# Kernel optimization log

Hardware: AMD Instinct MI355X
Metric: run time of the kernel (lower is better)

Reference implementation:

```python
import jax, jax.numpy as jnp
import numpy as np

N = 100000
E = 1600000
IN = 128
HID = 128
OUT = 40
EPS = 1e-5
NEG_SLOPE = 0.2


def _gat_layer(x, src, dst, W, a_src, a_dst, b, heads, out_dim):
    # x: [N, in]; W: [in, heads*out_dim]; a_src/a_dst: [heads, out_dim]; b: [heads*out_dim]
    n = x.shape[0]
    h = (x @ W).reshape(n, heads, out_dim)                      # [N, H, D]
    al_s = jnp.sum(h * a_src, axis=-1)                          # [N, H]
    al_d = jnp.sum(h * a_dst, axis=-1)                          # [N, H]
    e = jax.nn.leaky_relu(al_s[src] + al_d[dst], NEG_SLOPE)     # [E, H]
    m = jax.ops.segment_max(e, dst, num_segments=n)             # [N, H]
    m = jnp.where(jnp.isfinite(m), m, 0.0)
    ex = jnp.exp(e - m[dst])                                    # [E, H]
    denom = jax.ops.segment_sum(ex, dst, num_segments=n)        # [N, H]
    alpha = ex / (denom[dst] + 1e-16)                           # [E, H]
    out = jax.ops.segment_sum(alpha[:, :, None] * h[src], dst, num_segments=n)  # [N, H, D]
    return out.reshape(n, heads * out_dim) + b


def _bn(h, g, beta):
    mu = jnp.mean(h, axis=0)
    var = jnp.var(h, axis=0)
    return (h - mu) * jax.lax.rsqrt(var + EPS) * g + beta


def setup_inputs() -> dict:
    key = jax.random.key(0)
    ks = jax.random.split(key, 20)
    x = jax.random.normal(ks[0], (N, IN), dtype=jnp.float32)
    edge_index = jax.random.randint(ks[1], (2, E), 0, N, dtype=jnp.int64)
    s = 0.05
    d0 = HID // 2  # 64, heads=2
    return {
        "x": x,
        "edge_index": edge_index,
        "w0": jax.random.normal(ks[2], (IN, 2 * d0), jnp.float32) * s,
        "asrc0": jax.random.normal(ks[3], (2, d0), jnp.float32) * s,
        "adst0": jax.random.normal(ks[4], (2, d0), jnp.float32) * s,
        "b0": jnp.zeros((2 * d0,), jnp.float32),
        "g0": jnp.ones((2 * d0,), jnp.float32),
        "beta0": jnp.zeros((2 * d0,), jnp.float32),
        "w1": jax.random.normal(ks[5], (HID, 2 * d0), jnp.float32) * s,
        "asrc1": jax.random.normal(ks[6], (2, d0), jnp.float32) * s,
        "adst1": jax.random.normal(ks[7], (2, d0), jnp.float32) * s,
        "b1": jnp.zeros((2 * d0,), jnp.float32),
        "g1": jnp.ones((2 * d0,), jnp.float32),
        "beta1": jnp.zeros((2 * d0,), jnp.float32),
        "w2": jax.random.normal(ks[8], (HID, OUT), jnp.float32) * s,
        "asrc2": jax.random.normal(ks[9], (1, OUT), jnp.float32) * s,
        "adst2": jax.random.normal(ks[10], (1, OUT), jnp.float32) * s,
        "b2": jnp.zeros((OUT,), jnp.float32),
    }


def reference(x, edge_index, w0, asrc0, adst0, b0, g0, beta0,
              w1, asrc1, adst1, b1, g1, beta1,
              w2, asrc2, adst2, b2):
    src, dst = edge_index[0], edge_index[1]
    d0 = HID // 2
    # layer 0: GATConv(IN, 64, heads=2) -> BN -> ReLU (dropout off in eval)
    h = _gat_layer(x, src, dst, w0, asrc0, adst0, b0, 2, d0)
    h = jax.nn.relu(_bn(h, g0, beta0))
    # layer 1
    h = _gat_layer(h, src, dst, w1, asrc1, adst1, b1, 2, d0)
    h = jax.nn.relu(_bn(h, g1, beta1))
    # layer 2: GATConv(HID, OUT, heads=1), no bn/relu
    h = _gat_layer(h, src, dst, w2, asrc2, adst2, b2, 1, OUT)
    return h
```

## Files before the change

kernel.cpp:

```cpp
#include <hip/hip_runtime.h>
#include <cstdint>


#define TILE_A 8192
#define BCAP 10240
#define NSLICE 32

typedef __attribute__((ext_vector_type(8))) short bf16x8v;
typedef __attribute__((ext_vector_type(4))) float f32x4v;
typedef __attribute__((ext_vector_type(2))) float f32x2;
typedef __attribute__((ext_vector_type(2))) unsigned int u32x2;

__device__ __forceinline__ uint32_t bf16x2_pack(float a, float b) {
  uint32_t ua = __float_as_uint(a);
  ua = (ua + 0x7FFF + ((ua >> 16) & 1)) >> 16;
  uint32_t ub = __float_as_uint(b);
  ub = (ub + 0x7FFF + ((ub >> 16) & 1)) >> 16;
  return ua | (ub << 16);
}
__device__ __forceinline__ uint16_t bf16_1(float a) {
  uint32_t ua = __float_as_uint(a);
  return (uint16_t)((ua + 0x7FFF + ((ua >> 16) & 1)) >> 16);
}
__device__ __forceinline__ f32x2 up2(uint32_t u) {
  u32x2 t = {u << 16, u & 0xFFFF0000u};
  return __builtin_bit_cast(f32x2, t);
}


__global__ __launch_bounds__(256) void bucket_hist_k(const int* __restrict__ dst,
                                                     int* __restrict__ counts,
                                                     int E, int nbA, int nbuck) {
  __shared__ int hist[256];
  int t = threadIdx.x;
  hist[t] = 0;
  __syncthreads();
  int lo = blockIdx.x * TILE_A;
  int hi = min(lo + TILE_A, E);
  for (int i = lo + t; i < hi; i += 256) atomicAdd(&hist[dst[i] >> 9], 1);
  __syncthreads();
  if (t < nbuck) counts[t * nbA + blockIdx.x] = hist[t];
}

__global__ __launch_bounds__(1024) void scan_counts_k(int* __restrict__ counts, int M,
                                                      int* __restrict__ rowptr, int N, int E) {
  __shared__ int part[1024];
  int t = threadIdx.x;
  int chunk = (M + 1023) >> 10;
  int lo = t * chunk, hi = min(lo + chunk, M);
  int s = 0;
  for (int i = lo; i < hi; ++i) s += counts[i];
  part[t] = s;
  __syncthreads();
  for (int off = 1; off < 1024; off <<= 1) {
    int u = (t >= off) ? part[t - off] : 0;
    __syncthreads();
    part[t] += u;
    __syncthreads();
  }
  int run = (t == 0) ? 0 : part[t - 1];
  for (int i = lo; i < hi; ++i) {
    int v = counts[i];
    counts[i] = run;
    run += v;
  }
  if (t == 0) rowptr[N] = E;
}

__global__ __launch_bounds__(256) void bucket_scatter_k(const int* __restrict__ src,
                                                        const int* __restrict__ dst,
                                                        const int* __restrict__ counts,
                                                        uint32_t* __restrict__ barr,
                                                        int E, int nbA, int nbuck) {
  __shared__ int cur[256];
  int t = threadIdx.x;
  if (t < nbuck) cur[t] = counts[t * nbA + blockIdx.x];
  __syncthreads();
  int lo = blockIdx.x * TILE_A;
  int hi = min(lo + TILE_A, E);
  for (int i = lo + t; i < hi; i += 256) {
    int d = dst[i];
    int b = d >> 9;
    int pos = atomicAdd(&cur[b], 1);
    barr[pos] = ((uint32_t)(d & 511) << 17) | (uint32_t)src[i];
  }
}

__global__ __launch_bounds__(256) void bucket_sort_k(const uint32_t* __restrict__ barr,
                                                     const int* __restrict__ counts,
                                                     int* __restrict__ rowptr,
                                                     int* __restrict__ csr_src,
                                                     int nbA, int nbuck, int N, int E) {
  __shared__ uint32_t ebuf[BCAP];
  __shared__ int hist[512];
  __shared__ int cur[512];
  int b = blockIdx.x;
  int t = threadIdx.x;
  int start = counts[b * nbA];
  int end = (b == nbuck - 1) ? E : counts[(b + 1) * nbA];
  int cnt = end - start;
  if (cnt > BCAP) cnt = BCAP;
  for (int i = t; i < cnt; i += 256) ebuf[i] = barr[start + i];
  for (int i = t; i < 512; i += 256) hist[i] = 0;
  __syncthreads();
  for (int i = t; i < cnt; i += 256) atomicAdd(&hist[ebuf[i] >> 17], 1);
  __syncthreads();
  if (t < 64) {
    int v[8];
    int s = 0;
#pragma unroll
    for (int k = 0; k < 8; ++k) { v[k] = hist[t * 8 + k]; s += v[k]; }
    int inc = s;
#pragma unroll
    for (int off = 1; off < 64; off <<= 1) {
      int u = __shfl_up(inc, off, 64);
      if (t >= off) inc += u;
    }
    int run = inc - s;
#pragma unroll
    for (int k = 0; k < 8; ++k) { hist[t * 8 + k] = run; run += v[k]; }
  }
  __syncthreads();
  int node0 = b << 9;
  int lim = N - node0;
  if (lim > 512) lim = 512;
  for (int i = t; i < 512; i += 256) {
    cur[i] = hist[i];
    if (i < lim) rowptr[node0 + i] = start + hist[i];
  }
  __syncthreads();
  for (int i = t; i < cnt; i += 256) {
    uint32_t e = ebuf[i];
    int ld = e >> 17;
    int pos = atomicAdd(&cur[ld], 1);
    csr_src[start + pos] = (int)(e & 0x1FFFFu);
  }
}


__global__ void w_prep_all_k(const float* __restrict__ w0, const float* __restrict__ w1,
                             const float* __restrict__ w2, uint16_t* __restrict__ wt0,
                             uint16_t* __restrict__ wt1, uint16_t* __restrict__ wt2) {
  int idx = blockIdx.x * blockDim.x + threadIdx.x;
  if (idx < 16384) {
    int n = idx >> 7, k = idx & 127;
    wt0[idx] = bf16_1(w0[k * 128 + n]);
  } else if (idx < 32768) {
    int i = idx - 16384;
    int n = i >> 7, k = i & 127;
    wt1[i] = bf16_1(w1[k * 128 + n]);
  } else if (idx < 32768 + 48 * 128) {
    int i = idx - 32768;
    int n = i >> 7, k = i & 127;
    float v = (n < 40) ? w2[k * 40 + n] : 0.f;
    wt2[i] = bf16_1(v);
  }
}

template <bool NORM, int NT, int HEADS>
__global__ __launch_bounds__(256) void gemm_mfma_k(const float* __restrict__ X,
                                                   const uint16_t* __restrict__ WT,
                                                   uint16_t* __restrict__ Hout,
                                                   const float* __restrict__ stats,
                                                   const float* __restrict__ g,
                                                   const float* __restrict__ beta,
                                                   const float* __restrict__ asrc,
                                                   const float* __restrict__ adst,
                                                   float* __restrict__ als,
                                                   float* __restrict__ ald,
                                                   int nrows, int cols, int stride) {
  __shared__ short A_lds[64 * 136];
  __shared__ float sscale[128];
  __shared__ float sbias[128];
  int tid = threadIdx.x;
  if (NORM && tid < 128) {
    float s = 0.f, s2 = 0.f;
#pragma unroll 4
    for (int sl = 0; sl < NSLICE; ++sl) {
      s += stats[sl * 256 + tid];
      s2 += stats[sl * 256 + 128 + tid];
    }
    float invn = 1.0f / (float)nrows;
    float mean = s * invn;
    float var = s2 * invn - mean * mean;
    float sc = g[tid] * rsqrtf(var + 1e-5f);
    sscale[tid] = sc;
    sbias[tid] = beta[tid] - mean * sc;
  }
  if (NORM) __syncthreads();
  int row0 = blockIdx.x * 64;
#pragma unroll
  for (int it = 0; it < 8; ++it) {
    int e = (tid + it * 256) * 4;
    int row = e >> 7;
    int kh = e & 127;
    int gr = row0 + row;
    f32x4v xv = {0.f, 0.f, 0.f, 0.f};
    if (gr < nrows) xv = __builtin_nontemporal_load((const f32x4v*)(X + (size_t)gr * 128 + kh));
    if (NORM) {
      xv[0] = fmaxf(fmaf(xv[0], sscale[kh + 0], sbias[kh + 0]), 0.f);
      xv[1] = fmaxf(fmaf(xv[1], sscale[kh + 1], sbias[kh + 1]), 0.f);
      xv[2] = fmaxf(fmaf(xv[2], sscale[kh + 2], sbias[kh + 2]), 0.f);
      xv[3] = fmaxf(fmaf(xv[3], sscale[kh + 3], sbias[kh + 3]), 0.f);
    }
    uint2 pk;
    pk.x = bf16x2_pack(xv[0], xv[1]);
    pk.y = bf16x2_pack(xv[2], xv[3]);
    *(uint2*)(&A_lds[row * 136 + kh]) = pk;
  }
  __syncthreads();

  int wave = tid >> 6;
  int lane = tid & 63;
  int m = lane & 15;
  int quad = lane >> 4;

  bf16x8v afrag[4];
#pragma unroll
  for (int kc = 0; kc < 4; ++kc)
    afrag[kc] = *(const bf16x8v*)(&A_lds[(wave * 16 + m) * 136 + kc * 32 + quad * 8]);

  f32x4v acc[NT];
#pragma unroll
  for (int t = 0; t < NT; ++t) acc[t] = (f32x4v){0.f, 0.f, 0.f, 0.f};

#pragma unroll
  for (int t = 0; t < NT; ++t) {
#pragma unroll
    for (int kc = 0; kc < 4; ++kc) {
      bf16x8v bfrag = *(const bf16x8v*)(WT + ((t * 16 + m) * 128 + kc * 32 + quad * 8));
      acc[t] = __builtin_amdgcn_mfma_f32_16x16x32_bf16(afrag[kc], bfrag, acc[t], 0, 0, 0);
    }
  }

#pragma unroll
  for (int t = 0; t < NT; ++t) {
    int col = t * 16 + m;
    if (col >= cols) break;
#pragma unroll
    for (int r = 0; r < 4; ++r) {
      int row = row0 + wave * 16 + quad * 4 + r;
      if (row < nrows) Hout[(size_t)row * stride + col] = bf16_1(acc[t][r]);
    }
  }

  float as_v[NT], ad_v[NT];
#pragma unroll
  for (int t = 0; t < NT; ++t) {
    int col = t * 16 + m;
    as_v[t] = (col < cols) ? asrc[col] : 0.f;
    ad_v[t] = (col < cols) ? adst[col] : 0.f;
  }
#pragma unroll
  for (int r = 0; r < 4; ++r) {
    int row = row0 + wave * 16 + quad * 4 + r;
    if (HEADS == 2) {
      float s1h0 = 0.f, s2h0 = 0.f, s1h1 = 0.f, s2h1 = 0.f;
#pragma unroll
      for (int t = 0; t < NT / 2; ++t) {
        s1h0 += acc[t][r] * as_v[t];
        s2h0 += acc[t][r] * ad_v[t];
      }
#pragma unroll
      for (int t = NT / 2; t < NT; ++t) {
        s1h1 += acc[t][r] * as_v[t];
        s2h1 += acc[t][r] * ad_v[t];
      }
#pragma unroll
      for (int off = 1; off < 16; off <<= 1) {
        s1h0 += __shfl_xor(s1h0, off, 64);
        s2h0 += __shfl_xor(s2h0, off, 64);
        s1h1 += __shfl_xor(s1h1, off, 64);
        s2h1 += __shfl_xor(s2h1, off, 64);
      }
      if (m == 0 && row < nrows) {
        ((float2*)als)[row] = make_float2(s1h0, s1h1);
        ((float2*)ald)[row] = make_float2(s2h0, s2h1);
      }
    } else {
      float s1 = 0.f, s2 = 0.f;
#pragma unroll
      for (int t = 0; t < NT; ++t) {
        s1 += acc[t][r] * as_v[t];
        s2 += acc[t][r] * ad_v[t];
      }
#pragma unroll
      for (int off = 1; off < 16; off <<= 1) {
        s1 += __shfl_xor(s1, off, 64);
        s2 += __shfl_xor(s2, off, 64);
      }
      if (m == 0 && row < nrows) {
        als[row] = s1;
        ald[row] = s2;
      }
    }
  }
}

__global__ __launch_bounds__(256) void gat_gather2_k(const int* __restrict__ rowptr,
                                                     const int* __restrict__ csr_src,
                                                     const float* __restrict__ als,
                                                     const float* __restrict__ ald,
                                                     const uint16_t* __restrict__ H,
                                                     const float* __restrict__ bias,
                                                     float* __restrict__ out,
                                                     float* __restrict__ stats, int N) {
  __shared__ float red[4][256];
  int tid = threadIdx.x;
  int wv = tid >> 6;
  int n = blockIdx.x * 4 + wv;
  int lane = tid & 63;
  int slot = lane >> 4;
  int sub = lane & 15;
  int head = sub >> 3;
  bool alive = n < N;
  int start = 0, end = 0;
  float aldn = 0.f;
  if (alive) {
    start = rowptr[n];
    end = rowptr[n + 1];
    aldn = ald[2 * n + head];
  }
  const char* hbase = (const char*)H;
  uint32_t suboff = (uint32_t)sub << 4;
  bool dlane = (sub & 7) == 0;
  f32x2 acc0 = {0.f, 0.f}, acc1 = {0.f, 0.f}, acc2 = {0.f, 0.f}, acc3 = {0.f, 0.f};
  float dsum = 0.f;
  int j = start;
  for (; j + 16 <= end; j += 16) {
    int e0 = j + slot;
    int s0 = __builtin_nontemporal_load(csr_src + e0);
    int s1 = __builtin_nontemporal_load(csr_src + e0 + 4);
    int s2 = __builtin_nontemporal_load(csr_src + e0 + 8);
    int s3 = __builtin_nontemporal_load(csr_src + e0 + 12);
    uint4 u0 = *(const uint4*)(hbase + (((uint32_t)s0 << 8) + suboff));
    uint4 u1 = *(const uint4*)(hbase + (((uint32_t)s1 << 8) + suboff));
    uint4 u2 = *(const uint4*)(hbase + (((uint32_t)s2 << 8) + suboff));
    uint4 u3 = *(const uint4*)(hbase + (((uint32_t)s3 << 8) + suboff));
    float l0 = als[2 * s0 + head] + aldn;
    float l1 = als[2 * s1 + head] + aldn;
    float l2 = als[2 * s2 + head] + aldn;
    float l3 = als[2 * s3 + head] + aldn;
    l0 = fmaxf(l0, 0.2f * l0);
    l1 = fmaxf(l1, 0.2f * l1);
    l2 = fmaxf(l2, 0.2f * l2);
    l3 = fmaxf(l3, 0.2f * l3);
    float w0 = __expf(l0), w1 = __expf(l1), w2 = __expf(l2), w3 = __expf(l3);
    if (dlane) dsum += (w0 + w1) + (w2 + w3);
    acc0 += up2(u0.x) * w0;
    acc1 += up2(u0.y) * w0;
    acc2 += up2(u0.z) * w0;
    acc3 += up2(u0.w) * w0;
    acc0 += up2(u1.x) * w1;
    acc1 += up2(u1.y) * w1;
    acc2 += up2(u1.z) * w1;
    acc3 += up2(u1.w) * w1;
    acc0 += up2(u2.x) * w2;
    acc1 += up2(u2.y) * w2;
    acc2 += up2(u2.z) * w2;
    acc3 += up2(u2.w) * w2;
    acc0 += up2(u3.x) * w3;
    acc1 += up2(u3.y) * w3;
    acc2 += up2(u3.z) * w3;
    acc3 += up2(u3.w) * w3;
  }
  for (; j < end; j += 8) {
    int last = end - 1;
    int ea = j + slot;
    int eb = ea + 4;
    int sa = csr_src[min(ea, last)];
    int sb = csr_src[min(eb, last)];
    uint4 ua = *(const uint4*)(hbase + (((uint32_t)sa << 8) + suboff));
    uint4 ub = *(const uint4*)(hbase + (((uint32_t)sb << 8) + suboff));
    float la = als[2 * sa + head] + aldn;
    float lb = als[2 * sb + head] + aldn;
    la = fmaxf(la, 0.2f * la);
    lb = fmaxf(lb, 0.2f * lb);
    float wa = (ea < end) ? __expf(la) : 0.f;
    float wb = (eb < end) ? __expf(lb) : 0.f;
    if (dlane) dsum += wa + wb;
    acc0 += up2(ua.x) * wa;
    acc1 += up2(ua.y) * wa;
    acc2 += up2(ua.z) * wa;
    acc3 += up2(ua.w) * wa;
    acc0 += up2(ub.x) * wb;
    acc1 += up2(ub.y) * wb;
    acc2 += up2(ub.z) * wb;
    acc3 += up2(ub.w) * wb;
  }
  acc0.x += __shfl_xor(acc0.x, 16, 64); acc0.x += __shfl_xor(acc0.x, 32, 64);
  acc0.y += __shfl_xor(acc0.y, 16, 64); acc0.y += __shfl_xor(acc0.y, 32, 64);
  acc1.x += __shfl_xor(acc1.x, 16, 64); acc1.x += __shfl_xor(acc1.x, 32, 64);
  acc1.y += __shfl_xor(acc1.y, 16, 64); acc1.y += __shfl_xor(acc1.y, 32, 64);
  acc2.x += __shfl_xor(acc2.x, 16, 64); acc2.x += __shfl_xor(acc2.x, 32, 64);
  acc2.y += __shfl_xor(acc2.y, 16, 64); acc2.y += __shfl_xor(acc2.y, 32, 64);
  acc3.x += __shfl_xor(acc3.x, 16, 64); acc3.x += __shfl_xor(acc3.x, 32, 64);
  acc3.y += __shfl_xor(acc3.y, 16, 64); acc3.y += __shfl_xor(acc3.y, 32, 64);
  dsum += __shfl_xor(dsum, 16, 64);
  dsum += __shfl_xor(dsum, 32, 64);
  float denom = __shfl(dsum, head << 3, 64);
  float inv = 1.0f / (denom + 1e-16f);
  if (slot == 0) {
    float4 b0 = ((const float4*)bias)[2 * sub];
    float4 b1 = ((const float4*)bias)[2 * sub + 1];
    f32x4v o0, o1;
    o0[0] = acc0.x * inv + b0.x;
    o0[1] = acc0.y * inv + b0.y;
    o0[2] = acc1.x * inv + b0.z;
    o0[3] = acc1.y * inv + b0.w;
    o1[0] = acc2.x * inv + b1.x;
    o1[1] = acc2.y * inv + b1.y;
    o1[2] = acc3.x * inv + b1.z;
    o1[3] = acc3.y * inv + b1.w;
    if (alive) {
      float* orow = out + (size_t)n * 128 + 8 * sub;
      __builtin_nontemporal_store(o0, (f32x4v*)orow);
      __builtin_nontemporal_store(o1, (f32x4v*)(orow + 4));
    }
    float z = alive ? 1.f : 0.f;
    int c = sub << 3;
    red[wv][c + 0] = o0[0] * z;  red[wv][128 + c + 0] = o0[0] * o0[0] * z;
    red[wv][c + 1] = o0[1] * z;  red[wv][128 + c + 1] = o0[1] * o0[1] * z;
    red[wv][c + 2] = o0[2] * z;  red[wv][128 + c + 2] = o0[2] * o0[2] * z;
    red[wv][c + 3] = o0[3] * z;  red[wv][128 + c + 3] = o0[3] * o0[3] * z;
    red[wv][c + 4] = o1[0] * z;  red[wv][128 + c + 4] = o1[0] * o1[0] * z;
    red[wv][c + 5] = o1[1] * z;  red[wv][128 + c + 5] = o1[1] * o1[1] * z;
    red[wv][c + 6] = o1[2] * z;  red[wv][128 + c + 6] = o1[2] * o1[2] * z;
    red[wv][c + 7] = o1[3] * z;  red[wv][128 + c + 7] = o1[3] * o1[3] * z;
  }
  __syncthreads();
  float v = red[0][tid] + red[1][tid] + red[2][tid] + red[3][tid];
  atomicAdd(&stats[((blockIdx.x & (NSLICE - 1)) << 8) + tid], v);
}

__global__ __launch_bounds__(256) void gat_gather1_k(const int* __restrict__ rowptr,
                                                     const int* __restrict__ csr_src,
                                                     const float* __restrict__ als,
                                                     const float* __restrict__ ald,
                                                     const uint16_t* __restrict__ H,
                                                     const float* __restrict__ bias,
                                                     float* __restrict__ out, int N) {
  int n = blockIdx.x * 4 + (threadIdx.x >> 6);
  if (n >= N) return;
  int lane = threadIdx.x & 63;
  int slot = lane / 5;
  int d = lane - slot * 5;
  bool act = slot < 12;
  int start = rowptr[n], end = rowptr[n + 1];
  float aldn = ald[n];
  const char* hbase = (const char*)H;
  uint32_t doff = (uint32_t)d << 4;
  f32x2 a0 = {0.f, 0.f}, a1 = {0.f, 0.f}, a2 = {0.f, 0.f}, a3 = {0.f, 0.f};
  float dsum = 0.f;
  for (int j = start; j < end; j += 24) {
    int last = end - 1;
    int e0 = j + slot;
    int e1 = e0 + 12;
    int s0 = act ? __builtin_nontemporal_load(csr_src + min(e0, last)) : 0;
    int s1 = act ? __builtin_nontemporal_load(csr_src + min(e1, last)) : 0;
    uint4 u0 = *(const uint4*)(hbase + (((uint32_t)s0 << 7) + doff));
    uint4 u1 = *(const uint4*)(hbase + (((uint32_t)s1 << 7) + doff));
    float l0 = als[s0] + aldn;
    float l1 = als[s1] + aldn;
    l0 = fmaxf(l0, 0.2f * l0);
    l1 = fmaxf(l1, 0.2f * l1);
    float w0 = (act && e0 < end) ? __expf(l0) : 0.f;
    float w1 = (act && e1 < end) ? __expf(l1) : 0.f;
    if (d == 0) dsum += w0 + w1;
    a0 += up2(u0.x) * w0;
    a1 += up2(u0.y) * w0;
    a2 += up2(u0.z) * w0;
    a3 += up2(u0.w) * w0;
    a0 += up2(u1.x) * w1;
    a1 += up2(u1.y) * w1;
    a2 += up2(u1.z) * w1;
    a3 += up2(u1.w) * w1;
  }
#define FOLD2(off)                                        \
  a0.x += __shfl(a0.x, (lane + off) & 63, 64);            \
  a0.y += __shfl(a0.y, (lane + off) & 63, 64);            \
  a1.x += __shfl(a1.x, (lane + off) & 63, 64);            \
  a1.y += __shfl(a1.y, (lane + off) & 63, 64);            \
  a2.x += __shfl(a2.x, (lane + off) & 63, 64);            \
  a2.y += __shfl(a2.y, (lane + off) & 63, 64);            \
  a3.x += __shfl(a3.x, (lane + off) & 63, 64);            \
  a3.y += __shfl(a3.y, (lane + off) & 63, 64);
  FOLD2(30)
  FOLD2(15)
  {
    float t;
    t = __shfl(a0.x, (lane + 5) & 63, 64) + __shfl(a0.x, (lane + 10) & 63, 64); a0.x += t;
    t = __shfl(a0.y, (lane + 5) & 63, 64) + __shfl(a0.y, (lane + 10) & 63, 64); a0.y += t;
    t = __shfl(a1.x, (lane + 5) & 63, 64) + __shfl(a1.x, (lane + 10) & 63, 64); a1.x += t;
    t = __shfl(a1.y, (lane + 5) & 63, 64) + __shfl(a1.y, (lane + 10) & 63, 64); a1.y += t;
    t = __shfl(a2.x, (lane + 5) & 63, 64) + __shfl(a2.x, (lane + 10) & 63, 64); a2.x += t;
    t = __shfl(a2.y, (lane + 5) & 63, 64) + __shfl(a2.y, (lane + 10) & 63, 64); a2.y += t;
    t = __shfl(a3.x, (lane + 5) & 63, 64) + __shfl(a3.x, (lane + 10) & 63, 64); a3.x += t;
    t = __shfl(a3.y, (lane + 5) & 63, 64) + __shfl(a3.y, (lane + 10) & 63, 64); a3.y += t;
  }
#undef FOLD2
#pragma unroll
  for (int off = 1; off < 64; off <<= 1) dsum += __shfl_xor(dsum, off, 64);
  if (lane < 5) {
    float inv = 1.0f / (dsum + 1e-16f);
    float4 b4a = ((const float4*)bias)[2 * d];
    float4 b4b = ((const float4*)bias)[2 * d + 1];
    f32x4v o0, o1;
    o0[0] = a0.x * inv + b4a.x;
    o0[1] = a0.y * inv + b4a.y;
    o0[2] = a1.x * inv + b4a.z;
    o0[3] = a1.y * inv + b4a.w;
    o1[0] = a2.x * inv + b4b.x;
    o1[1] = a2.y * inv + b4b.y;
    o1[2] = a3.x * inv + b4b.z;
    o1[3] = a3.y * inv + b4b.w;
    float* orow = out + (size_t)n * 40 + 8 * d;
    __builtin_nontemporal_store(o0, (f32x4v*)orow);
    __builtin_nontemporal_store(o1, (f32x4v*)(orow + 4));
  }
}

extern "C" void kernel_launch(void* const* d_in, const int* in_sizes, int n_in,
                              void* d_out, int out_size, void* d_ws, size_t ws_size,
                              hipStream_t stream) {
  const float* x     = (const float*)d_in[0];
  const int*   ei    = (const int*)d_in[1];
  const float* w0    = (const float*)d_in[2];
  const float* asrc0 = (const float*)d_in[3];
  const float* adst0 = (const float*)d_in[4];
  const float* b0    = (const float*)d_in[5];
  const float* g0    = (const float*)d_in[6];
  const float* beta0 = (const float*)d_in[7];
  const float* w1    = (const float*)d_in[8];
  const float* asrc1 = (const float*)d_in[9];
  const float* adst1 = (const float*)d_in[10];
  const float* b1    = (const float*)d_in[11];
  const float* g1    = (const float*)d_in[12];
  const float* beta1 = (const float*)d_in[13];
  const float* w2    = (const float*)d_in[14];
  const float* asrc2 = (const float*)d_in[15];
  const float* adst2 = (const float*)d_in[16];
  const float* b2    = (const float*)d_in[17];

  const int N = in_sizes[0] / 128;
  const int E = in_sizes[1] / 2;

  const int nbuck = (N + 511) >> 9;
  const int nbA = (E + TILE_A - 1) / TILE_A;

  char* p = (char*)d_ws;
  auto carve = [&](size_t bytes) {
    char* q = p;
    p += (bytes + 255) & ~(size_t)255;
    return q;
  };
  int*      counts  = (int*)carve((size_t)nbuck * nbA * 4);
  int*      rowptr  = (int*)carve((size_t)(N + 1) * 4);
  uint32_t* barr    = (uint32_t*)carve((size_t)E * 4);
  int*      csr_src = (int*)carve((size_t)E * 4);
  float*    als     = (float*)carve((size_t)N * 2 * 4);
  float*    ald     = (float*)carve((size_t)N * 2 * 4);
  float*    stats   = (float*)carve((size_t)2 * NSLICE * 256 * 4);
  uint16_t* wt0     = (uint16_t*)carve(128 * 128 * 2);
  uint16_t* wt1     = (uint16_t*)carve(128 * 128 * 2);
  uint16_t* wt2     = (uint16_t*)carve(48 * 128 * 2);
  uint16_t* hbuf    = (uint16_t*)carve((size_t)N * 128 * 2);
  float*    agg     = (float*)carve((size_t)N * 128 * 4);

  float* stats0 = stats;
  float* stats1 = stats + NSLICE * 256;

  const int* esrc = ei;
  const int* edst = ei + E;

  bucket_hist_k<<<nbA, 256, 0, stream>>>(edst, counts, E, nbA, nbuck);
  scan_counts_k<<<1, 1024, 0, stream>>>(counts, nbuck * nbA, rowptr, N, E);
  bucket_scatter_k<<<nbA, 256, 0, stream>>>(esrc, edst, counts, barr, E, nbA, nbuck);
  bucket_sort_k<<<nbuck, 256, 0, stream>>>(barr, counts, rowptr, csr_src, nbA, nbuck, N, E);

  w_prep_all_k<<<(32768 + 48 * 128 + 255) / 256, 256, 0, stream>>>(w0, w1, w2, wt0, wt1, wt2);
  hipMemsetAsync(stats, 0, 2 * NSLICE * 256 * 4, stream);

  const int gemm_grid = (N + 63) / 64;
  const int node_grid = (N + 3) / 4;

  gemm_mfma_k<false, 8, 2><<<gemm_grid, 256, 0, stream>>>(x, wt0, hbuf, nullptr, nullptr,
                                                          nullptr, asrc0, adst0, als, ald,
                                                          N, 128, 128);
  gat_gather2_k<<<node_grid, 256, 0, stream>>>(rowptr, csr_src, als, ald, hbuf,
                                               b0, agg, stats0, N);

  gemm_mfma_k<true, 8, 2><<<gemm_grid, 256, 0, stream>>>(agg, wt1, hbuf, stats0, g0, beta0,
                                                         asrc1, adst1, als, ald, N, 128, 128);
  gat_gather2_k<<<node_grid, 256, 0, stream>>>(rowptr, csr_src, als, ald, hbuf,
                                               b1, agg, stats1, N);

  gemm_mfma_k<true, 3, 1><<<gemm_grid, 256, 0, stream>>>(agg, wt2, hbuf, stats1, g1, beta1,
                                                         asrc2, adst2, als, ald, N, 40, 64);
  gat_gather1_k<<<node_grid, 256, 0, stream>>>(rowptr, csr_src, als, ald, hbuf,
                                               b2, (float*)d_out, N);
}
```

Before: 525.5 us.

## Stage GEMM output in LDS for coalesced stores and use finer CSR buckets

The GEMM epilogue now writes its bf16 results into LDS and then stores them to global memory with 16-byte vector writes, replacing scattered 2-byte stores. The attention logits are computed from the rounded bf16 values held in LDS, reduced per row through a small shared array. Separately, the CSR build uses 256-node buckets with smaller edge tiles, which means more blocks and less LDS per sort block. The logits are now taken from bf16-rounded values rather than fp32 accumulators, which changes numerics slightly, and the extra syncs and LDS traffic add cost.

After: 949.3 us. 80.7% more time.

```diff
diff --git a/kernel.cpp b/kernel.cpp
--- a/kernel.cpp
+++ b/kernel.cpp
@@ -2,14 +2,15 @@
 #include <cstdint>
 
 
-#define TILE_A 8192
-#define BCAP 10240
+#define TILE_A 2048
+#define BCAP 6144
 #define NSLICE 32
 
 typedef __attribute__((ext_vector_type(8))) short bf16x8v;
 typedef __attribute__((ext_vector_type(4))) float f32x4v;
 typedef __attribute__((ext_vector_type(2))) float f32x2;
 typedef __attribute__((ext_vector_type(2))) unsigned int u32x2;
+typedef __attribute__((ext_vector_type(4))) unsigned int u32x4;
 
 __device__ __forceinline__ uint32_t bf16x2_pack(float a, float b) {
   uint32_t ua = __float_as_uint(a);
@@ -31,15 +32,15 @@
 __global__ __launch_bounds__(256) void bucket_hist_k(const int* __restrict__ dst,
                                                      int* __restrict__ counts,
                                                      int E, int nbA, int nbuck) {
-  __shared__ int hist[256];
+  __shared__ int hist[512];
   int t = threadIdx.x;
-  hist[t] = 0;
+  for (int i = t; i < 512; i += 256) hist[i] = 0;
   __syncthreads();
   int lo = blockIdx.x * TILE_A;
   int hi = min(lo + TILE_A, E);
-  for (int i = lo + t; i < hi; i += 256) atomicAdd(&hist[dst[i] >> 9], 1);
-  __syncthreads();
-  if (t < nbuck) counts[t * nbA + blockIdx.x] = hist[t];
+  for (int i = lo + t; i < hi; i += 256) atomicAdd(&hist[dst[i] >> 8], 1);
+  __syncthreads();
+  for (int i = t; i < nbuck; i += 256) counts[i * nbA + blockIdx.x] = hist[i];
 }
 
 __global__ __launch_bounds__(1024) void scan_counts_k(int* __restrict__ counts, int M,
@@ -72,17 +73,17 @@
                                                         const int* __restrict__ counts,
                                                         uint32_t* __restrict__ barr,
                                                         int E, int nbA, int nbuck) {
-  __shared__ int cur[256];
+  __shared__ int cur[512];
   int t = threadIdx.x;
-  if (t < nbuck) cur[t] = counts[t * nbA + blockIdx.x];
+  for (int i = t; i < nbuck; i += 256) cur[i] = counts[i * nbA + blockIdx.x];
   __syncthreads();
   int lo = blockIdx.x * TILE_A;
   int hi = min(lo + TILE_A, E);
   for (int i = lo + t; i < hi; i += 256) {
     int d = dst[i];
-    int b = d >> 9;
+    int b = d >> 8;
     int pos = atomicAdd(&cur[b], 1);
-    barr[pos] = ((uint32_t)(d & 511) << 17) | (uint32_t)src[i];
+    barr[pos] = ((uint32_t)(d & 255) << 17) | (uint32_t)src[i];
   }
 }
 
@@ -92,8 +93,8 @@
                                                      int* __restrict__ csr_src,
                                                      int nbA, int nbuck, int N, int E) {
   __shared__ uint32_t ebuf[BCAP];
-  __shared__ int hist[512];
-  __shared__ int cur[512];
+  __shared__ int hist[256];
+  __shared__ int cur[256];
   int b = blockIdx.x;
   int t = threadIdx.x;
   int start = counts[b * nbA];
@@ -101,15 +102,15 @@
   int cnt = end - start;
   if (cnt > BCAP) cnt = BCAP;
   for (int i = t; i < cnt; i += 256) ebuf[i] = barr[start + i];
-  for (int i = t; i < 512; i += 256) hist[i] = 0;
+  if (t < 256) hist[t] = 0;
   __syncthreads();
   for (int i = t; i < cnt; i += 256) atomicAdd(&hist[ebuf[i] >> 17], 1);
   __syncthreads();
   if (t < 64) {
-    int v[8];
+    int v[4];
     int s = 0;
 #pragma unroll
-    for (int k = 0; k < 8; ++k) { v[k] = hist[t * 8 + k]; s += v[k]; }
+    for (int k = 0; k < 4; ++k) { v[k] = hist[t * 4 + k]; s += v[k]; }
     int inc = s;
 #pragma unroll
     for (int off = 1; off < 64; off <<= 1) {
@@ -118,15 +119,15 @@
     }
     int run = inc - s;
 #pragma unroll
-    for (int k = 0; k < 8; ++k) { hist[t * 8 + k] = run; run += v[k]; }
-  }
-  __syncthreads();
-  int node0 = b << 9;
+    for (int k = 0; k < 4; ++k) { hist[t * 4 + k] = run; run += v[k]; }
+  }
+  __syncthreads();
+  int node0 = b << 8;
   int lim = N - node0;
-  if (lim > 512) lim = 512;
-  for (int i = t; i < 512; i += 256) {
-    cur[i] = hist[i];
-    if (i < lim) rowptr[node0 + i] = start + hist[i];
+  if (lim > 256) lim = 256;
+  if (t < 256) {
+    cur[t] = hist[t];
+    if (t < lim) rowptr[node0 + t] = start + hist[t];
   }
   __syncthreads();
   for (int i = t; i < cnt; i += 256) {
@@ -172,7 +173,15 @@
   __shared__ short A_lds[64 * 136];
   __shared__ float sscale[128];
   __shared__ float sbias[128];
+  __shared__ float sasrc[128];
+  __shared__ float sadst[128];
+  __shared__ float part_s[64][4];
+  __shared__ float part_d[64][4];
   int tid = threadIdx.x;
+  if (tid < 128) {
+    sasrc[tid] = (tid < cols) ? asrc[tid] : 0.f;
+    sadst[tid] = (tid < cols) ? adst[tid] : 0.f;
+  }
   if (NORM && tid < 128) {
     float s = 0.f, s2 = 0.f;
 #pragma unroll 4
@@ -233,65 +242,69 @@
     }
   }
 
+  __syncthreads();
+  if (NT == 3) {
+    for (int i = tid; i < 64 * 16; i += 256) {
+      int row = i >> 4, c = 48 + (i & 15);
+      A_lds[row * 136 + c] = 0;
+    }
+  }
 #pragma unroll
   for (int t = 0; t < NT; ++t) {
     int col = t * 16 + m;
-    if (col >= cols) break;
 #pragma unroll
     for (int r = 0; r < 4; ++r) {
-      int row = row0 + wave * 16 + quad * 4 + r;
-      if (row < nrows) Hout[(size_t)row * stride + col] = bf16_1(acc[t][r]);
-    }
-  }
-
-  float as_v[NT], ad_v[NT];
-#pragma unroll
-  for (int t = 0; t < NT; ++t) {
-    int col = t * 16 + m;
-    as_v[t] = (col < cols) ? asrc[col] : 0.f;
-    ad_v[t] = (col < cols) ? adst[col] : 0.f;
-  }
-#pragma unroll
-  for (int r = 0; r < 4; ++r) {
-    int row = row0 + wave * 16 + quad * 4 + r;
-    if (HEADS == 2) {
-      float s1h0 = 0.f, s2h0 = 0.f, s1h1 = 0.f, s2h1 = 0.f;
-#pragma unroll
-      for (int t = 0; t < NT / 2; ++t) {
-        s1h0 += acc[t][r] * as_v[t];
-        s2h0 += acc[t][r] * ad_v[t];
+      int row = wave * 16 + quad * 4 + r;
+      A_lds[row * 136 + col] = (short)bf16_1(acc[t][r]);
+    }
+  }
+  __syncthreads();
+
+  constexpr int NCH = (NT == 8) ? 4 : 2;
+  if (tid < 64 * NCH) {
+    int row = tid / NCH, ch = tid % NCH;
+    float ps = 0.f, pd = 0.f;
+#pragma unroll
+    for (int q = 0; q < 4; ++q) {
+      bf16x8v hv = *(const bf16x8v*)(&A_lds[row * 136 + ch * 32 + q * 8]);
+#pragma unroll
+      for (int e = 0; e < 8; ++e) {
+        float hf = __uint_as_float(((uint32_t)(unsigned short)hv[e]) << 16);
+        int c = ch * 32 + q * 8 + e;
+        ps = fmaf(hf, sasrc[c], ps);
+        pd = fmaf(hf, sadst[c], pd);
       }
-#pragma unroll
-      for (int t = NT / 2; t < NT; ++t) {
-        s1h1 += acc[t][r] * as_v[t];
-        s2h1 += acc[t][r] * ad_v[t];
-      }
-#pragma unroll
-      for (int off = 1; off < 16; off <<= 1) {
-        s1h0 += __shfl_xor(s1h0, off, 64);
-        s2h0 += __shfl_xor(s2h0, off, 64);
-        s1h1 += __shfl_xor(s1h1, off, 64);
-        s2h1 += __shfl_xor(s2h1, off, 64);
-      }
-      if (m == 0 && row < nrows) {
-        ((float2*)als)[row] = make_float2(s1h0, s1h1);
-        ((float2*)ald)[row] = make_float2(s2h0, s2h1);
-      }
-    } else {
-      float s1 = 0.f, s2 = 0.f;
-#pragma unroll
-      for (int t = 0; t < NT; ++t) {
-        s1 += acc[t][r] * as_v[t];
-        s2 += acc[t][r] * ad_v[t];
-      }
-#pragma unroll
-      for (int off = 1; off < 16; off <<= 1) {
-        s1 += __shfl_xor(s1, off, 64);
-        s2 += __shfl_xor(s2, off, 64);
-      }
-      if (m == 0 && row < nrows) {
-        als[row] = s1;
-        ald[row] = s2;
+    }
+    part_s[row][ch] = ps;
+    part_d[row][ch] = pd;
+  }
+
+  int c8 = stride >> 3;
+  int total = 64 * c8;
+  for (int idx = tid; idx < total; idx += 256) {
+    int row = idx / c8;
+    int cc = (idx - row * c8) * 8;
+    int grow = row0 + row;
+    if (grow < nrows) {
+      u32x4 v = *(const u32x4*)(&A_lds[row * 136 + cc]);
+      *(u32x4*)(Hout + (size_t)grow * stride + cc) = v;
+    }
+  }
+
+  __syncthreads();
+  if (tid < 64) {
+    int grow = row0 + tid;
+    if (grow < nrows) {
+      if (HEADS == 2) {
+        float s0 = part_s[tid][0] + part_s[tid][1];
+        float s1 = part_s[tid][2] + part_s[tid][3];
+        float d0 = part_d[tid][0] + part_d[tid][1];
+        float d1 = part_d[tid][2] + part_d[tid][3];
+        ((float2*)als)[grow] = make_float2(s0, s1);
+        ((float2*)ald)[grow] = make_float2(d0, d1);
+      } else {
+        als[grow] = part_s[tid][0] + part_s[tid][1];
+        ald[grow] = part_d[tid][0] + part_d[tid][1];
       }
     }
   }
@@ -545,7 +558,7 @@
   const int N = in_sizes[0] / 128;
   const int E = in_sizes[1] / 2;
 
-  const int nbuck = (N + 511) >> 9;
+  const int nbuck = (N + 255) >> 8;
   const int nbA = (E + TILE_A - 1) / TILE_A;
 
   char* p = (char*)d_ws;
```
